# Kernel optimization log

Measured on AMD Instinct MI355X. Metric: run time of the kernel, lower is better.

## Reference

```python
import jax, jax.numpy as jnp
import numpy as np

SPATIAL_SHAPES = [(128, 128), (64, 64), (32, 32), (16, 16)]  # (H_l, W_l) per level
NUM_HEADS = 8
NUM_LEVELS = 4
NUM_POINTS = 4
EMBED_DIM = 256
HEAD_DIM = EMBED_DIM // NUM_HEADS
LEN_V = sum(h * w for h, w in SPATIAL_SHAPES)  # 21760
BS, LQ = 8, 900


def setup_inputs() -> dict:
    key = jax.random.key(0)
    ks = jax.random.split(key, 12)
    s = 0.05
    return {
        'query': jax.random.normal(ks[0], (BS, LQ, EMBED_DIM), jnp.float32),
        'reference_points': jax.random.uniform(ks[1], (BS, LQ, NUM_LEVELS, 2), jnp.float32),
        'value': jax.random.normal(ks[2], (BS, LEN_V, EMBED_DIM), jnp.float32),
        'w_value': jax.random.normal(ks[3], (EMBED_DIM, EMBED_DIM), jnp.float32) * s,
        'b_value': jnp.zeros((EMBED_DIM,), jnp.float32),
        'w_off': jax.random.normal(ks[4], (EMBED_DIM, NUM_HEADS * NUM_LEVELS * NUM_POINTS * 2), jnp.float32) * s,
        'b_off': jax.random.normal(ks[5], (NUM_HEADS * NUM_LEVELS * NUM_POINTS * 2,), jnp.float32),
        'w_attn': jax.random.normal(ks[6], (EMBED_DIM, NUM_HEADS * NUM_LEVELS * NUM_POINTS), jnp.float32) * s,
        'b_attn': jnp.zeros((NUM_HEADS * NUM_LEVELS * NUM_POINTS,), jnp.float32),
        'w_out': jax.random.normal(ks[7], (EMBED_DIM, EMBED_DIM), jnp.float32) * s,
        'b_out': jnp.zeros((EMBED_DIM,), jnp.float32),
    }


def _bilinear_sample(val, locx, locy, H, W):
    # val: [bs, nh, H*W, hd]; locx/locy: [bs, nh, N] normalized in [0,1]
    # grid_sample semantics: align_corners=False, zero padding.
    px = locx * W - 0.5
    py = locy * H - 0.5
    x0 = jnp.floor(px)
    y0 = jnp.floor(py)
    dx = px - x0
    dy = py - y0
    x0i = x0.astype(jnp.int32)
    y0i = y0.astype(jnp.int32)
    out = jnp.zeros(val.shape[:2] + (locx.shape[-1], val.shape[-1]), val.dtype)
    corners = [
        (x0i, y0i, (1 - dx) * (1 - dy)),
        (x0i + 1, y0i, dx * (1 - dy)),
        (x0i, y0i + 1, (1 - dx) * dy),
        (x0i + 1, y0i + 1, dx * dy),
    ]
    for xi, yi, w in corners:
        valid = ((xi >= 0) & (xi < W) & (yi >= 0) & (yi < H)).astype(val.dtype)
        idx = jnp.clip(yi, 0, H - 1) * W + jnp.clip(xi, 0, W - 1)
        g = jnp.take_along_axis(val, idx[..., None], axis=2)  # [bs,nh,N,hd]
        out = out + g * (w * valid)[..., None]
    return out


def reference(query, reference_points, value, w_value, b_value, w_off, b_off,
              w_attn, b_attn, w_out, b_out):
    bs, Lq, C = query.shape
    # value projection -> [bs, Lv, nh, hd]
    v = (value @ w_value + b_value).reshape(bs, -1, NUM_HEADS, HEAD_DIM)
    # sampling offsets [bs,Lq,nh,L,P,2], attention weights softmax over L*P
    off = (query @ w_off + b_off).reshape(bs, Lq, NUM_HEADS, NUM_LEVELS, NUM_POINTS, 2)
    aw = (query @ w_attn + b_attn).reshape(bs, Lq, NUM_HEADS, NUM_LEVELS * NUM_POINTS)
    aw = jax.nn.softmax(aw, axis=-1).reshape(bs, Lq, NUM_HEADS, NUM_LEVELS, NUM_POINTS)
    # normalizer is (W_l, H_l) per level (flip of spatial shapes)
    norm = jnp.asarray([[w, h] for h, w in SPATIAL_SHAPES], query.dtype)  # [L,2]
    loc = reference_points[:, :, None, :, None, :] + off / norm[None, None, None, :, None, :]
    # per-level bilinear sampling and weighted reduction
    out = jnp.zeros((bs, Lq, NUM_HEADS, HEAD_DIM), query.dtype)
    start = 0
    for l, (H, W) in enumerate(SPATIAL_SHAPES):
        vl = v[:, start:start + H * W]                       # [bs,HW,nh,hd]
        vl = vl.transpose(0, 2, 1, 3)                        # [bs,nh,HW,hd]
        ll = loc[:, :, :, l].transpose(0, 2, 1, 3, 4)        # [bs,nh,Lq,P,2]
        ll = ll.reshape(bs, NUM_HEADS, Lq * NUM_POINTS, 2)
        s = _bilinear_sample(vl, ll[..., 0], ll[..., 1], H, W)
        s = s.reshape(bs, NUM_HEADS, Lq, NUM_POINTS, HEAD_DIM)
        out = out + jnp.einsum('bhqpd,bqhp->bqhd', s, aw[:, :, :, l])
        start += H * W
    out = out.reshape(bs, Lq, C)
    return out @ w_out + b_out
```

## Files before the change

kernel.cpp:

```cpp
#include <hip/hip_runtime.h>

#define BS 8
#define LQ 900
#define NH 8
#define NL 4
#define NP 4
#define HD 32
#define ED 256
#define LEN_V 21760

typedef __attribute__((ext_vector_type(8))) short bf16x8;
typedef __attribute__((ext_vector_type(4))) float f32x4;
typedef __attribute__((ext_vector_type(4))) float fv4;

static __device__ __forceinline__ unsigned short f2bf(float f) {
  union { float f; unsigned u; } x; x.f = f;
  unsigned r = x.u + 0x7fffu + ((x.u >> 16) & 1u);
  return (unsigned short)(r >> 16);
}
static __device__ __forceinline__ float bf_lo(unsigned u) {
  union { unsigned u; float f; } x; x.u = u << 16;
  return x.f;
}
static __device__ __forceinline__ float bf_hi(unsigned u) {
  union { unsigned u; float f; } x; x.u = u & 0xffff0000u;
  return x.f;
}
static __device__ __forceinline__ unsigned pack2(float a, float b) {
  return (unsigned)f2bf(a) | ((unsigned)f2bf(b) << 16);
}

__global__ __launch_bounds__(256) void bprep_kernel(
    const float* __restrict__ w, unsigned short* __restrict__ Bsw) {
  const int id = blockIdx.x * 256 + threadIdx.x;
  const int n = id & 255;
  const int kseg = (id >> 8) & 3;
  const int kc = id >> 10;
  const float* src = &w[(kc * 32 + kseg * 8) * 256 + n];
  float f[8];
#pragma unroll
  for (int j = 0; j < 8; j++) f[j] = src[j * 256];
  uint4 pk;
  pk.x = pack2(f[0], f[1]);
  pk.y = pack2(f[2], f[3]);
  pk.z = pack2(f[4], f[5]);
  pk.w = pack2(f[6], f[7]);
  *(uint4*)&Bsw[((kc * 4 + kseg) * 256 + n) * 8] = pk;
}

__global__ __launch_bounds__(256, 4) void vproj_kernel(
    const float* __restrict__ value, const unsigned short* __restrict__ Bsw,
    const float* __restrict__ bias, unsigned short* __restrict__ vout) {
  const int t = threadIdx.x;
  const int row0 = blockIdx.x * 64;
  const int wv = t >> 6;
  const int lane = t & 63;
  const int quad = lane >> 4;
  const int nn = lane & 15;

  __shared__ unsigned short a_lds[4 * 64 * 8];

  f32x4 acc[4][4];
#pragma unroll
  for (int i = 0; i < 4; i++)
#pragma unroll
    for (int j = 0; j < 4; j++) acc[i][j] = (f32x4)(0.f);

  const int arow = t >> 2;
  const int akseg = t & 3;
  const unsigned short* bptr = &Bsw[(quad * 256 + wv * 64 + nn) * 8];

  for (int kc = 0; kc < 8; kc++) {
    __syncthreads();
    {
      const float* pa = &value[(row0 + arow) * 256 + kc * 32 + akseg * 8];
      fv4 v0 = __builtin_nontemporal_load((const fv4*)pa);
      fv4 v1 = __builtin_nontemporal_load((const fv4*)(pa + 4));
      uint4 pk;
      pk.x = pack2(v0.x, v0.y);
      pk.y = pack2(v0.z, v0.w);
      pk.z = pack2(v1.x, v1.y);
      pk.w = pack2(v1.z, v1.w);
      *(uint4*)&a_lds[(akseg * 64 + arow) * 8] = pk;
    }
    __syncthreads();

    bf16x8 af[4], bfr[4];
#pragma unroll
    for (int ct = 0; ct < 4; ct++)
      bfr[ct] = *(const bf16x8*)(bptr + (kc * 1024 + ct * 16) * 8);
#pragma unroll
    for (int rt = 0; rt < 4; rt++)
      af[rt] = *(const bf16x8*)&a_lds[(quad * 64 + rt * 16 + nn) * 8];
#pragma unroll
    for (int rt = 0; rt < 4; rt++)
#pragma unroll
      for (int ct = 0; ct < 4; ct++)
        acc[rt][ct] = __builtin_amdgcn_mfma_f32_16x16x32_bf16(
            af[rt], bfr[ct], acc[rt][ct], 0, 0, 0);
  }

  const int bb = row0 / LEN_V;
  const int s0 = row0 - bb * LEN_V;
#pragma unroll
  for (int ct = 0; ct < 4; ct++) {
    const int col = wv * 64 + ct * 16 + nn;
    const float bv = bias[col];
    const int h = col >> 5;
    const int d = col & 31;
    unsigned short* vb = &vout[((bb * NH + h) * LEN_V + s0) * HD + d];
#pragma unroll
    for (int rt = 0; rt < 4; rt++) {
      f32x4 f = acc[rt][ct];
#pragma unroll
      for (int reg = 0; reg < 4; reg++) {
        const int s = rt * 16 + quad * 4 + reg;
        vb[s * HD] = f2bf(f[reg] + bv);
      }
    }
  }
}

__global__ __launch_bounds__(384, 2) void offattn_kernel(
    const float* __restrict__ query,
    const float* __restrict__ w_off, const float* __restrict__ b_off,
    const float* __restrict__ w_attn, const float* __restrict__ b_attn,
    float* __restrict__ OFF, float* __restrict__ LOG) {
  const int t = threadIdx.x;
  const int row0 = blockIdx.x * 32;
  const int rg = t / 96;
  const int c4 = t % 96;
  const int col = c4 * 4;
  const bool isOff = col < 256;
  const float* wbase = isOff ? (w_off + col) : (w_attn + (col - 256));
  const int wstride = isOff ? 256 : 128;
  const float* bb = isOff ? (b_off + col) : (b_attn + (col - 256));
  __shared__ float a_lds[32][8];

  float4 acc[8];
#pragma unroll
  for (int r = 0; r < 8; r++) acc[r] = make_float4(0.f, 0.f, 0.f, 0.f);

  for (int k0 = 0; k0 < 256; k0 += 8) {
    __syncthreads();
    if (t < 256) a_lds[t >> 3][t & 7] = query[(row0 + (t >> 3)) * 256 + k0 + (t & 7)];
    __syncthreads();
    float4 wr[8];
#pragma unroll
    for (int k = 0; k < 8; k++)
      wr[k] = *(const float4*)&wbase[(k0 + k) * wstride];
#pragma unroll
    for (int r = 0; r < 8; r++) {
      const float* ar = &a_lds[rg * 8 + r][0];
      float4 a0 = *(const float4*)&ar[0];
      float4 a1 = *(const float4*)&ar[4];
      float4 s = acc[r];
      s.x += a0.x*wr[0].x + a0.y*wr[1].x + a0.z*wr[2].x + a0.w*wr[3].x
           + a1.x*wr[4].x + a1.y*wr[5].x + a1.z*wr[6].x + a1.w*wr[7].x;
      s.y += a0.x*wr[0].y + a0.y*wr[1].y + a0.z*wr[2].y + a0.w*wr[3].y
           + a1.x*wr[4].y + a1.y*wr[5].y + a1.z*wr[6].y + a1.w*wr[7].y;
      s.z += a0.x*wr[0].z + a0.y*wr[1].z + a0.z*wr[2].z + a0.w*wr[3].z
           + a1.x*wr[4].z + a1.y*wr[5].z + a1.z*wr[6].z + a1.w*wr[7].z;
      s.w += a0.x*wr[0].w + a0.y*wr[1].w + a0.z*wr[2].w + a0.w*wr[3].w
           + a1.x*wr[4].w + a1.y*wr[5].w + a1.z*wr[6].w + a1.w*wr[7].w;
      acc[r] = s;
    }
  }

  const float4 bv = *(const float4*)bb;
#pragma unroll
  for (int r = 0; r < 8; r++) {
    const int grow = row0 + rg * 8 + r;
    float4 o = make_float4(acc[r].x + bv.x, acc[r].y + bv.y,
                           acc[r].z + bv.z, acc[r].w + bv.w);
    if (isOff) *(float4*)&OFF[grow * 256 + col] = o;
    else       *(float4*)&LOG[grow * 128 + (col - 256)] = o;
  }
}

__global__ __launch_bounds__(256, 6) void sample_kernel(
    const float* __restrict__ refp, const unsigned short* __restrict__ vp,
    const float* __restrict__ OFF, const float* __restrict__ LOG,
    float* __restrict__ RES) {
  const int t = threadIdx.x;
  const int b = blockIdx.x / (LQ / 4);
  const int q0 = (blockIdx.x % (LQ / 4)) * 4;

  __shared__ float off_lds[4][256];
  __shared__ float aw_lds[4][128];
  __shared__ float ref_lds[4][4][2];
  __shared__ int   soff[512][4];
  __shared__ float swt[512][4];

#pragma unroll
  for (int qi = 0; qi < 4; qi++)
    off_lds[qi][t] = OFF[(b * LQ + q0 + qi) * 256 + t];
  if (t < 128) {
#pragma unroll
    for (int qi = 0; qi < 4; qi++)
      aw_lds[qi][t] = LOG[(b * LQ + q0 + qi) * 128 + t];
  }
  if (t < 32) {
    const int qi = t >> 3, l = (t >> 1) & 3, xy = t & 1;
    ref_lds[qi][l][xy] = refp[((b * LQ + q0 + qi) * NL + l) * 2 + xy];
  }
  __syncthreads();

  if (t < 32) {
    const int qi = t >> 3, h = t & 7;
    float* a = &aw_lds[qi][h * 16];
    float m = a[0];
#pragma unroll
    for (int i = 1; i < 16; i++) m = fmaxf(m, a[i]);
    float e[16];
    float ssum = 0.f;
#pragma unroll
    for (int i = 0; i < 16; i++) { e[i] = __expf(a[i] - m); ssum += e[i]; }
    const float inv = 1.f / ssum;
#pragma unroll
    for (int i = 0; i < 16; i++) a[i] = e[i] * inv;
  }
  __syncthreads();

#pragma unroll
  for (int ss = 0; ss < 2; ss++) {
    const int sid = t + ss * 256;
    const int p = sid & 3, l = (sid >> 2) & 3, h = (sid >> 4) & 7, qi = sid >> 7;
    const int W = 128 >> l;
    const int base = (l == 0) ? 0 : ((l == 1) ? 16384 : ((l == 2) ? 20480 : 21504));
    const float Wf = (float)W;
    const float refx = ref_lds[qi][l][0];
    const float refy = ref_lds[qi][l][1];
    const float offx = off_lds[qi][h * 32 + l * 8 + p * 2 + 0];
    const float offy = off_lds[qi][h * 32 + l * 8 + p * 2 + 1];
    const float aw = aw_lds[qi][h * 16 + l * 4 + p];
    const float px = refx * Wf + offx - 0.5f;
    const float py = refy * Wf + offy - 0.5f;
    const float x0f = floorf(px), y0f = floorf(py);
    const float dx = px - x0f, dy = py - y0f;
    const int x0 = (int)x0f, y0 = (int)y0f;
    const int x1 = x0 + 1, y1 = y0 + 1;
    const float mx0 = (x0 >= 0 && x0 < W) ? 1.f : 0.f;
    const float mx1 = (x1 >= 0 && x1 < W) ? 1.f : 0.f;
    const float my0 = (y0 >= 0 && y0 < W) ? 1.f : 0.f;
    const float my1 = (y1 >= 0 && y1 < W) ? 1.f : 0.f;
    const int x0c = min(max(x0, 0), W - 1);
    const int x1c = min(max(x1, 0), W - 1);
    const int y0c = min(max(y0, 0), W - 1);
    const int y1c = min(max(y1, 0), W - 1);
    soff[sid][0] = (base + y0c * W + x0c) * 8;
    soff[sid][1] = (base + y0c * W + x1c) * 8;
    soff[sid][2] = (base + y1c * W + x0c) * 8;
    soff[sid][3] = (base + y1c * W + x1c) * 8;
    swt[sid][0] = (1.f - dx) * (1.f - dy) * mx0 * my0 * aw;
    swt[sid][1] = dx * (1.f - dy) * mx1 * my0 * aw;
    swt[sid][2] = (1.f - dx) * dy * mx0 * my1 * aw;
    swt[sid][3] = dx * dy * mx1 * my1 * aw;
  }
  __syncthreads();

  const int qi = t >> 6;
  const int hh = (t >> 3) & 7;
  const int d4 = t & 7;
  const uint2* vpu2 = (const uint2*)vp + (size_t)(b * NH + hh) * (LEN_V * HD / 4);
  float r0 = 0.f, r1 = 0.f, r2 = 0.f, r3 = 0.f;
  const int sbase = (qi * 8 + hh) << 4;
#pragma unroll 4
  for (int lp = 0; lp < 16; lp++) {
    const int sid = sbase + lp;
    const int4 o = *(const int4*)&soff[sid][0];
    const float4 w = *(const float4*)&swt[sid][0];
    const uint2 u00 = vpu2[o.x + d4];
    const uint2 u10 = vpu2[o.y + d4];
    const uint2 u01 = vpu2[o.z + d4];
    const uint2 u11 = vpu2[o.w + d4];
    r0 += w.x * bf_lo(u00.x) + w.y * bf_lo(u10.x) + w.z * bf_lo(u01.x) + w.w * bf_lo(u11.x);
    r1 += w.x * bf_hi(u00.x) + w.y * bf_hi(u10.x) + w.z * bf_hi(u01.x) + w.w * bf_hi(u11.x);
    r2 += w.x * bf_lo(u00.y) + w.y * bf_lo(u10.y) + w.z * bf_lo(u01.y) + w.w * bf_lo(u11.y);
    r3 += w.x * bf_hi(u00.y) + w.y * bf_hi(u10.y) + w.z * bf_hi(u01.y) + w.w * bf_hi(u11.y);
  }
  float4 rr = make_float4(r0, r1, r2, r3);
  *(float4*)&RES[(b * LQ + q0 + qi) * 256 + hh * 32 + d4 * 4] = rr;
}

__global__ __launch_bounds__(256, 2) void outproj_kernel(
    const float* __restrict__ RES, const float* __restrict__ w,
    const float* __restrict__ bias, float* __restrict__ out) {
  const int t = threadIdx.x;
  const int row0 = blockIdx.x * 32;
  const int rg = t >> 6;
  const int c0 = (t & 63) << 2;
  __shared__ float a_lds[32][8];

  float4 acc[8];
#pragma unroll
  for (int r = 0; r < 8; r++) acc[r] = make_float4(0.f, 0.f, 0.f, 0.f);

  const int lr = t >> 3;
  const int lk = t & 7;
  for (int k0 = 0; k0 < 256; k0 += 8) {
    __syncthreads();
    a_lds[lr][lk] = RES[(row0 + lr) * 256 + k0 + lk];
    __syncthreads();
    float4 wr[8];
#pragma unroll
    for (int k = 0; k < 8; k++)
      wr[k] = *(const float4*)&w[(k0 + k) * 256 + c0];
#pragma unroll
    for (int r = 0; r < 8; r++) {
      const float* ar = &a_lds[rg * 8 + r][0];
      float4 a0 = *(const float4*)&ar[0];
      float4 a1 = *(const float4*)&ar[4];
      float4 s = acc[r];
      s.x += a0.x*wr[0].x + a0.y*wr[1].x + a0.z*wr[2].x + a0.w*wr[3].x
           + a1.x*wr[4].x + a1.y*wr[5].x + a1.z*wr[6].x + a1.w*wr[7].x;
      s.y += a0.x*wr[0].y + a0.y*wr[1].y + a0.z*wr[2].y + a0.w*wr[3].y
           + a1.x*wr[4].y + a1.y*wr[5].y + a1.z*wr[6].y + a1.w*wr[7].y;
      s.z += a0.x*wr[0].z + a0.y*wr[1].z + a0.z*wr[2].z + a0.w*wr[3].z
           + a1.x*wr[4].z + a1.y*wr[5].z + a1.z*wr[6].z + a1.w*wr[7].z;
      s.w += a0.x*wr[0].w + a0.y*wr[1].w + a0.z*wr[2].w + a0.w*wr[3].w
           + a1.x*wr[4].w + a1.y*wr[5].w + a1.z*wr[6].w + a1.w*wr[7].w;
      acc[r] = s;
    }
  }

  const float4 bv = *(const float4*)&bias[c0];
#pragma unroll
  for (int r = 0; r < 8; r++) {
    const int grow = row0 + rg * 8 + r;
    float4 o = make_float4(acc[r].x + bv.x, acc[r].y + bv.y,
                           acc[r].z + bv.z, acc[r].w + bv.w);
    *(float4*)&out[grow * 256 + c0] = o;
  }
}

extern "C" void kernel_launch(void* const* d_in, const int* in_sizes, int n_in,
                              void* d_out, int out_size, void* d_ws, size_t ws_size,
                              hipStream_t stream) {
  (void)in_sizes; (void)n_in; (void)out_size; (void)ws_size;
  const float* query   = (const float*)d_in[0];
  const float* refp    = (const float*)d_in[1];
  const float* value   = (const float*)d_in[2];
  const float* w_value = (const float*)d_in[3];
  const float* b_value = (const float*)d_in[4];
  const float* w_off   = (const float*)d_in[5];
  const float* b_off   = (const float*)d_in[6];
  const float* w_attn  = (const float*)d_in[7];
  const float* b_attn  = (const float*)d_in[8];
  const float* w_out   = (const float*)d_in[9];
  const float* b_out   = (const float*)d_in[10];
  float* out = (float*)d_out;

  char* ws = (char*)d_ws;
  unsigned short* vp = (unsigned short*)ws;
  float* OFF = (float*)(ws + 89128960);
  float* LOG = (float*)(ws + 89128960 + 7372800);
  float* RES = (float*)(ws + 89128960 + 7372800 + 3686400);
  unsigned short* Bsw = (unsigned short*)(ws + 89128960 + 7372800 + 3686400 + 7372800);

  bprep_kernel<<<32, 256, 0, stream>>>(w_value, Bsw);
  vproj_kernel<<<(BS * LEN_V) / 64, 256, 0, stream>>>(value, Bsw, b_value, vp);
  offattn_kernel<<<(BS * LQ) / 32, 384, 0, stream>>>(query, w_off, b_off,
                                                     w_attn, b_attn, OFF, LOG);
  sample_kernel<<<BS * (LQ / 4), 256, 0, stream>>>(refp, vp, OFF, LOG, RES);
  outproj_kernel<<<(BS * LQ) / 32, 256, 0, stream>>>(RES, w_out, b_out, out);
}
```

Before: 422.6 us.

## Double-buffer value projection LDS and widen sampling gathers with split corner pairs

```diff
diff --git a/kernel.cpp b/kernel.cpp
--- a/kernel.cpp
+++ b/kernel.cpp
@@ -58,7 +58,7 @@
   const int quad = lane >> 4;
   const int nn = lane & 15;
 
-  __shared__ unsigned short a_lds[4 * 64 * 8];
+  __shared__ unsigned short a_lds[2][4 * 64 * 8];
 
   f32x4 acc[4][4];
 #pragma unroll
@@ -68,36 +68,51 @@
 
   const int arow = t >> 2;
   const int akseg = t & 3;
+  const int aslot = (akseg * 64 + arow) * 8;
   const unsigned short* bptr = &Bsw[(quad * 256 + wv * 64 + nn) * 8];
+  const float* abase = &value[(row0 + arow) * 256 + akseg * 8];
+
+  {
+    fv4 v0 = __builtin_nontemporal_load((const fv4*)abase);
+    fv4 v1 = __builtin_nontemporal_load((const fv4*)(abase + 4));
+    uint4 pk;
+    pk.x = pack2(v0.x, v0.y);
+    pk.y = pack2(v0.z, v0.w);
+    pk.z = pack2(v1.x, v1.y);
+    pk.w = pack2(v1.z, v1.w);
+    *(uint4*)&a_lds[0][aslot] = pk;
+  }
 
   for (int kc = 0; kc < 8; kc++) {
     __syncthreads();
-    {
-      const float* pa = &value[(row0 + arow) * 256 + kc * 32 + akseg * 8];
-      fv4 v0 = __builtin_nontemporal_load((const fv4*)pa);
-      fv4 v1 = __builtin_nontemporal_load((const fv4*)(pa + 4));
-      uint4 pk;
-      pk.x = pack2(v0.x, v0.y);
-      pk.y = pack2(v0.z, v0.w);
-      pk.z = pack2(v1.x, v1.y);
-      pk.w = pack2(v1.z, v1.w);
-      *(uint4*)&a_lds[(akseg * 64 + arow) * 8] = pk;
-    }
-    __syncthreads();
-
+    fv4 n0, n1;
+    if (kc < 7) {
+      const float* pa = abase + (kc + 1) * 32;
+      n0 = __builtin_nontemporal_load((const fv4*)pa);
+      n1 = __builtin_nontemporal_load((const fv4*)(pa + 4));
+    }
     bf16x8 af[4], bfr[4];
 #pragma unroll
     for (int ct = 0; ct < 4; ct++)
       bfr[ct] = *(const bf16x8*)(bptr + (kc * 1024 + ct * 16) * 8);
+    const unsigned short* cur = &a_lds[kc & 1][0];
 #pragma unroll
     for (int rt = 0; rt < 4; rt++)
-      af[rt] = *(const bf16x8*)&a_lds[(quad * 64 + rt * 16 + nn) * 8];
+      af[rt] = *(const bf16x8*)&cur[(quad * 64 + rt * 16 + nn) * 8];
 #pragma unroll
     for (int rt = 0; rt < 4; rt++)
 #pragma unroll
       for (int ct = 0; ct < 4; ct++)
         acc[rt][ct] = __builtin_amdgcn_mfma_f32_16x16x32_bf16(
             af[rt], bfr[ct], acc[rt][ct], 0, 0, 0);
+    if (kc < 7) {
+      uint4 pk;
+      pk.x = pack2(n0.x, n0.y);
+      pk.y = pack2(n0.z, n0.w);
+      pk.z = pack2(n1.x, n1.y);
+      pk.w = pack2(n1.z, n1.w);
+      *(uint4*)&a_lds[(kc + 1) & 1][aslot] = pk;
+    }
   }
 
   const int bb = row0 / LEN_V;
@@ -183,14 +198,13 @@
     const float* __restrict__ OFF, const float* __restrict__ LOG,
     float* __restrict__ RES) {
   const int t = threadIdx.x;
-  const int b = blockIdx.x / (LQ / 4);
-  const int q0 = (blockIdx.x % (LQ / 4)) * 4;
+  const int b = blockIdx.x & 7;
+  const int q0 = (blockIdx.x >> 3) * 4;
 
   __shared__ float off_lds[4][256];
   __shared__ float aw_lds[4][128];
   __shared__ float ref_lds[4][4][2];
-  __shared__ int   soff[512][4];
-  __shared__ float swt[512][4];
+  __shared__ int scw[1024][4];
 
 #pragma unroll
   for (int qi = 0; qi < 4; qi++)
@@ -248,39 +262,52 @@
     const int x1c = min(max(x1, 0), W - 1);
     const int y0c = min(max(y0, 0), W - 1);
     const int y1c = min(max(y1, 0), W - 1);
-    soff[sid][0] = (base + y0c * W + x0c) * 8;
-    soff[sid][1] = (base + y0c * W + x1c) * 8;
-    soff[sid][2] = (base + y1c * W + x0c) * 8;
-    soff[sid][3] = (base + y1c * W + x1c) * 8;
-    swt[sid][0] = (1.f - dx) * (1.f - dy) * mx0 * my0 * aw;
-    swt[sid][1] = dx * (1.f - dy) * mx1 * my0 * aw;
-    swt[sid][2] = (1.f - dx) * dy * mx0 * my1 * aw;
-    swt[sid][3] = dx * dy * mx1 * my1 * aw;
+    const float w00 = (1.f - dx) * (1.f - dy) * mx0 * my0 * aw;
+    const float w10 = dx * (1.f - dy) * mx1 * my0 * aw;
+    const float w01 = (1.f - dx) * dy * mx0 * my1 * aw;
+    const float w11 = dx * dy * mx1 * my1 * aw;
+    const int slot = (((l * 4 + p) * 32) + qi * 8 + h) * 2;
+    int4 recA, recB;
+    recA.x = (base + y0c * W + x0c) * 4; recA.y = __float_as_int(w00);
+    recA.z = (base + y0c * W + x1c) * 4; recA.w = __float_as_int(w10);
+    recB.x = (base + y1c * W + x0c) * 4; recB.y = __float_as_int(w01);
+    recB.z = (base + y1c * W + x1c) * 4; recB.w = __float_as_int(w11);
+    *(int4*)&scw[slot + 0][0] = recA;
+    *(int4*)&scw[slot + 1][0] = recB;
   }
   __syncthreads();
 
   const int qi = t >> 6;
-  const int hh = (t >> 3) & 7;
-  const int d4 = t & 7;
-  const uint2* vpu2 = (const uint2*)vp + (size_t)(b * NH + hh) * (LEN_V * HD / 4);
-  float r0 = 0.f, r1 = 0.f, r2 = 0.f, r3 = 0.f;
-  const int sbase = (qi * 8 + hh) << 4;
+  const int lane = t & 63;
+  const int hh = lane >> 3;
+  const int d8 = (lane >> 1) & 3;
+  const int cp = lane & 1;
+  const uint4* vpu = (const uint4*)vp + (size_t)(b * NH + hh) * (LEN_V * HD / 8);
+  float r[8];
+#pragma unroll
+  for (int j = 0; j < 8; j++) r[j] = 0.f;
+  const int sbase = (qi * 8 + hh) * 2 + cp;
 #pragma unroll 4
   for (int lp = 0; lp < 16; lp++) {
-    const int sid = sbase + lp;
-    const int4 o = *(const int4*)&soff[sid][0];
-    const float4 w = *(const float4*)&swt[sid][0];
-    const uint2 u00 = vpu2[o.x + d4];
-    const uint2 u10 = vpu2[o.y + d4];
-    const uint2 u01 = vpu2[o.z + d4];
-    const uint2 u11 = vpu2[o.w + d4];
-    r0 += w.x * bf_lo(u00.x) + w.y * bf_lo(u10.x) + w.z * bf_lo(u01.x) + w.w * bf_lo(u11.x);
-    r1 += w.x * bf_hi(u00.x) + w.y * bf_hi(u10.x) + w.z * bf_hi(u01.x) + w.w * bf_hi(u11.x);
-    r2 += w.x * bf_lo(u00.y) + w.y * bf_lo(u10.y) + w.z * bf_lo(u01.y) + w.w * bf_lo(u11.y);
-    r3 += w.x * bf_hi(u00.y) + w.y * bf_hi(u10.y) + w.z * bf_hi(u01.y) + w.w * bf_hi(u11.y);
-  }
-  float4 rr = make_float4(r0, r1, r2, r3);
-  *(float4*)&RES[(b * LQ + q0 + qi) * 256 + hh * 32 + d4 * 4] = rr;
+    const int4 rec = *(const int4*)&scw[lp * 64 + sbase][0];
+    const uint4 ua = vpu[rec.x + d8];
+    const uint4 ub = vpu[rec.z + d8];
+    const float wa = __int_as_float(rec.y);
+    const float wb = __int_as_float(rec.w);
+    r[0] += wa * bf_lo(ua.x) + wb * bf_lo(ub.x);
+    r[1] += wa * bf_hi(ua.x) + wb * bf_hi(ub.x);
+    r[2] += wa * bf_lo(ua.y) + wb * bf_lo(ub.y);
+    r[3] += wa * bf_hi(ua.y) + wb * bf_hi(ub.y);
+    r[4] += wa * bf_lo(ua.z) + wb * bf_lo(ub.z);
+    r[5] += wa * bf_hi(ua.z) + wb * bf_hi(ub.z);
+    r[6] += wa * bf_lo(ua.w) + wb * bf_lo(ub.w);
+    r[7] += wa * bf_hi(ua.w) + wb * bf_hi(ub.w);
+  }
+#pragma unroll
+  for (int j = 0; j < 8; j++) r[j] += __shfl_xor(r[j], 1);
+  float4 o = cp ? make_float4(r[4], r[5], r[6], r[7])
+               : make_float4(r[0], r[1], r[2], r[3]);
+  *(float4*)&RES[(b * LQ + q0 + qi) * 256 + hh * 32 + d8 * 8 + cp * 4] = o;
 }
 
 __global__ __launch_bounds__(256, 2) void outproj_kernel(
```

Result: no change. 425.3 us (+0.6%).
